# Kernel tuning notes

Measured on AMD Instinct MI355X. Metric: run time of the kernel, lower is better.

## Reference

```python
import jax, jax.numpy as jnp
import numpy as np

SEG = 2048      # segment_length
RATE = 4        # dilated_rate
DIM = 768
LN_EPS = 1e-5


def _sparsify(x):
    # b (l s) d -> b l s d, take every RATE-th within segment, flatten back
    b, L, d = x.shape
    x = x.reshape(b, L // SEG, SEG, d)[:, :, ::RATE]
    return x.reshape(b, -1, d)


def _layernorm(x, gamma, beta):
    mu = jnp.mean(x, axis=-1, keepdims=True)
    var = jnp.mean(jnp.square(x - mu), axis=-1, keepdims=True)
    return (x - mu) / jnp.sqrt(var + LN_EPS) * gamma + beta


def setup_inputs() -> dict:
    key = jax.random.key(0)
    ks = jax.random.split(key, 6)
    B, L, D = 4, 8192, DIM
    return {
        "Q": jax.random.normal(ks[0], (B, L, D), dtype=jnp.float32),
        "K": jax.random.normal(ks[1], (B, L, D), dtype=jnp.float32),
        "V": jax.random.normal(ks[2], (B, L, D), dtype=jnp.float32),
        "Wq": jax.random.normal(ks[3], (D, D), dtype=jnp.float32) * (1.0 / np.sqrt(D)),
        "Wk": jax.random.normal(ks[4], (D, D), dtype=jnp.float32) * (1.0 / np.sqrt(D)),
        "Wv": jax.random.normal(ks[5], (D, D), dtype=jnp.float32) * (1.0 / np.sqrt(D)),
        "ln_gamma": jnp.ones((D,), dtype=jnp.float32),
        "ln_beta": jnp.zeros((D,), dtype=jnp.float32),
    }


def reference(Q, K, V, Wq, Wk, Wv, ln_gamma, ln_beta):
    # strided segment dilation gather
    q = _sparsify(Q)  # [B, Ls, D], Ls = L/SEG * ceil(SEG/RATE)
    k = _sparsify(K)
    v = _sparsify(V)
    # linear projections (torch Linear: y = x @ W.T, no bias)
    q = q @ Wq.T
    k = k @ Wk.T
    v = v @ Wv.T
    # qk LayerNorm (shared norm module)
    q = _layernorm(q, ln_gamma, ln_beta)
    k = _layernorm(k, ln_gamma, ln_beta)
    # scaled dot product attention (non-causal, default scale 1/sqrt(D))
    scale = 1.0 / np.sqrt(q.shape[-1]).astype(np.float32)
    attn = jax.nn.softmax(jnp.einsum('bqd,bkd->bqk', q, k) * scale, axis=-1)
    out = jnp.einsum('bqk,bkd->bqd', attn, v)
    # dropout is identity in eval mode; final softmax over feature dim (as in source)
    return jax.nn.softmax(out, axis=-1)
```

## Files before the change

### kernel.cpp

```cpp
#include <hip/hip_runtime.h>
#include <math.h>

#define SEGLEN 2048
#define SRATE 4
#define DIM 768
#define BATCH 4
#define LFULL 8192
#define LSP 2048
#define NROWS (BATCH * LSP)
#define LN_EPS 1e-5f
#define ATT_SCALE 0.03608439182435161f

typedef __attribute__((ext_vector_type(8))) short s16x8;
typedef __attribute__((ext_vector_type(4))) float f32x4;

__device__ __forceinline__ ushort f2bf(float f) {
    unsigned u = __float_as_uint(f);
    u += 0x7fffu + ((u >> 16) & 1u);
    return (ushort)(u >> 16);
}
__device__ __forceinline__ float bf2f(ushort h) {
    return __uint_as_float(((unsigned)h) << 16);
}

__device__ __forceinline__ void ld_lds16(const ushort* g, ushort* l) {
    __builtin_amdgcn_global_load_lds(
        (const __attribute__((address_space(1))) void*)g,
        (__attribute__((address_space(3))) void*)l, 16, 0, 0);
}

__global__ void pack3(const float* __restrict__ Q, const float* __restrict__ Ks,
                      const float* __restrict__ V, ushort* __restrict__ X) {
    const float* src = blockIdx.z == 0 ? Q : blockIdx.z == 1 ? Ks : V;
    ushort* dst = X + (long)blockIdx.z * (NROWS * DIM);
    int idx = blockIdx.x * 256 + threadIdx.x;
    int r  = idx / (DIM / 4);
    int dg = idx - r * (DIM / 4);
    int bb = r >> 11;
    int s  = r & 2047;
    int seg = s >> 9;
    int j   = s & 511;
    long srow = (long)bb * LFULL + seg * SEGLEN + j * SRATE;
    float4 f = *(const float4*)(src + srow * DIM + dg * 4);
    ushort4 o;
    o.x = f2bf(f.x); o.y = f2bf(f.y); o.z = f2bf(f.z); o.w = f2bf(f.w);
    *(ushort4*)(dst + (long)r * DIM + dg * 4) = o;
}

__global__ void conv3(const float* __restrict__ Wq, const float* __restrict__ Wk,
                      const float* __restrict__ Wv, ushort* __restrict__ W) {
    const float* src = blockIdx.z == 0 ? Wq : blockIdx.z == 1 ? Wk : Wv;
    ushort* dst = W + (long)blockIdx.z * (DIM * DIM);
    int idx = blockIdx.x * 256 + threadIdx.x;
    float4 f = *(const float4*)(src + (long)idx * 4);
    ushort4 o;
    o.x = f2bf(f.x); o.y = f2bf(f.y); o.z = f2bf(f.z); o.w = f2bf(f.w);
    *(ushort4*)(dst + (long)idx * 4) = o;
}

#define GTILE 128
#define GBK 64

template<int MODE>
__global__ __launch_bounds__(256) void gemm_bt(
    const ushort* __restrict__ Ag, const ushort* __restrict__ Bg,
    ushort* __restrict__ Cb, ushort* __restrict__ Cb2,
    float* __restrict__ Cf, float* __restrict__ Cf2, float* __restrict__ lsum,
    int M, int N, int K, int lda, int ldb, long sA, long sB, long sC,
    int ldc, float scale)
{
    __shared__ ushort As[GTILE * GBK];
    __shared__ ushort Bs[GTILE * GBK];

    const int CT = gridDim.x, RT = gridDim.y;
    const int nt = CT * RT;
    const int total = nt * gridDim.z;
    int g = (blockIdx.z * RT + blockIdx.y) * CT + blockIdx.x;
    g = (g & 7) * (total >> 3) + (g >> 3);
    const int z = g / nt;
    const int rem = g - z * nt;
    const int by = rem / CT, bx = rem - by * CT;

    const int bz = (MODE == 3) ? (z >> 1) : z;
    const int hz = (MODE == 3) ? (z & 1) : 0;
    const ushort* A = Ag + (long)bz * sA + (long)hz * K;
    const ushort* B = Bg + (long)bz * sB + (long)hz * K;

    const int tid = threadIdx.x;
    const int rowBase = by * GTILE;
    const int colBase = bx * GTILE;
    const int wid = tid >> 6, lane = tid & 63;
    const int wm = wid >> 1, wn = wid & 1;
    const int quad = lane >> 4, lr = lane & 15;

    f32x4 acc[4][4] = {};

    const ushort* gA = A + (long)(rowBase + wid * 32 + (lane & 7)) * lda + (lane >> 3) * 8;
    const ushort* gB = B + (long)(colBase + wid * 32 + (lane & 7)) * ldb + (lane >> 3) * 8;
    ushort* lA = As + wid * 2048;
    ushort* lB = Bs + wid * 2048;

    const int fra = (wm * 8 + (lr >> 3)) * 512 + (lr & 7) * 8;
    const int frb = (wn * 8 + (lr >> 3)) * 512 + (lr & 7) * 8;

    for (int k0 = 0; k0 < K; k0 += GBK) {
        __syncthreads();
#pragma unroll
        for (int s = 0; s < 4; s++) {
            ld_lds16(gA + (long)s * 8 * lda + k0, lA + s * 512);
            ld_lds16(gB + (long)s * 8 * ldb + k0, lB + s * 512);
        }
        __syncthreads();

#pragma unroll
        for (int h = 0; h < 2; h++) {
            s16x8 af[4], bfm[4];
#pragma unroll
            for (int t = 0; t < 4; t++)
                af[t] = *(const s16x8*)&As[fra + t * 1024 + (h * 4 + quad) * 64];
#pragma unroll
            for (int t = 0; t < 4; t++)
                bfm[t] = *(const s16x8*)&Bs[frb + t * 1024 + (h * 4 + quad) * 64];
#pragma unroll
            for (int i = 0; i < 4; i++)
#pragma unroll
                for (int j = 0; j < 4; j++)
                    acc[i][j] = __builtin_amdgcn_mfma_f32_16x16x32_bf16(af[i], bfm[j], acc[i][j], 0, 0, 0);
        }
    }

    if (MODE == 0) {
        if (z < 2) {
            ushort* Cz = Cb + (long)z * sC;
#pragma unroll
            for (int i = 0; i < 4; i++) {
                int r0 = rowBase + wm * 64 + i * 16 + quad * 4;
#pragma unroll
                for (int j = 0; j < 4; j++) {
                    int c = colBase + wn * 64 + j * 16 + lr;
#pragma unroll
                    for (int reg = 0; reg < 4; reg++)
                        Cz[(long)(r0 + reg) * ldc + c] = f2bf(acc[i][j][reg]);
                }
            }
        } else {
#pragma unroll
            for (int i = 0; i < 4; i++) {
                int r0 = rowBase + wm * 64 + i * 16 + quad * 4;
                int bidx = r0 >> 11;
                int jj = r0 & 2047;
                ushort* Cz = Cb2 + (long)bidx * DIM * LSP;
#pragma unroll
                for (int j = 0; j < 4; j++) {
                    int c = colBase + wn * 64 + j * 16 + lr;
                    ushort4 o;
                    o.x = f2bf(acc[i][j][0]); o.y = f2bf(acc[i][j][1]);
                    o.z = f2bf(acc[i][j][2]); o.w = f2bf(acc[i][j][3]);
                    *(ushort4*)(Cz + (long)c * LSP + jj) = o;
                }
            }
        }
    } else if (MODE == 2) {
        ushort* Cz = Cb + (long)z * sC;
        float* lz = lsum + (long)z * M;
#pragma unroll
        for (int i = 0; i < 4; i++) {
            int r0 = rowBase + wm * 64 + i * 16 + quad * 4;
#pragma unroll
            for (int reg = 0; reg < 4; reg++) {
                float s = 0.f;
#pragma unroll
                for (int j = 0; j < 4; j++) {
                    int c = colBase + wn * 64 + j * 16 + lr;
                    float e = __expf(acc[i][j][reg] * scale);
                    s += e;
                    Cz[(long)(r0 + reg) * ldc + c] = f2bf(e);
                }
                for (int m = 1; m < 16; m <<= 1) s += __shfl_xor(s, m, 64);
                if (lr == 0) atomicAdd(&lz[r0 + reg], s);
            }
        }
    } else {
        float* Cz = (hz ? Cf2 : Cf) + (long)bz * sC;
#pragma unroll
        for (int i = 0; i < 4; i++) {
            int r0 = rowBase + wm * 64 + i * 16 + quad * 4;
#pragma unroll
            for (int j = 0; j < 4; j++) {
                int c = colBase + wn * 64 + j * 16 + lr;
#pragma unroll
                for (int reg = 0; reg < 4; reg++)
                    Cz[(long)(r0 + reg) * ldc + c] = acc[i][j][reg];
            }
        }
    }
}

__global__ __launch_bounds__(256) void ln_inplace(
    ushort* __restrict__ X, const float* __restrict__ gamma,
    const float* __restrict__ beta)
{
    int wid = threadIdx.x >> 6, lane = threadIdx.x & 63;
    int row = blockIdx.x * 4 + wid;
    ushort* xp = X + (long)row * DIM;
    float v[12];
    float s = 0.f;
#pragma unroll
    for (int c = 0; c < 12; c++) { v[c] = bf2f(xp[c * 64 + lane]); s += v[c]; }
    for (int m = 1; m < 64; m <<= 1) s += __shfl_xor(s, m, 64);
    float mean = s * (1.0f / 768.0f);
    float q = 0.f;
#pragma unroll
    for (int c = 0; c < 12; c++) { float d = v[c] - mean; q += d * d; }
    for (int m = 1; m < 64; m <<= 1) q += __shfl_xor(q, m, 64);
    float rstd = rsqrtf(q * (1.0f / 768.0f) + LN_EPS);
#pragma unroll
    for (int c = 0; c < 12; c++) {
        int idx = c * 64 + lane;
        float y = (v[c] - mean) * rstd * gamma[idx] + beta[idx];
        xp[idx] = f2bf(y);
    }
}

__global__ __launch_bounds__(256) void final_softmax(
    const float* __restrict__ O0, const float* __restrict__ O1,
    const float* __restrict__ l, float* __restrict__ out)
{
    int wid = threadIdx.x >> 6, lane = threadIdx.x & 63;
    int row = blockIdx.x * 4 + wid;
    long base = (long)row * DIM;
    float inv = 1.0f / l[row];
    float v[12]; float mx = -1e30f;
#pragma unroll
    for (int c = 0; c < 12; c++) {
        v[c] = (O0[base + c * 64 + lane] + O1[base + c * 64 + lane]) * inv;
        mx = fmaxf(mx, v[c]);
    }
    for (int m = 1; m < 64; m <<= 1) mx = fmaxf(mx, __shfl_xor(mx, m, 64));
    float s = 0.f;
#pragma unroll
    for (int c = 0; c < 12; c++) { v[c] = __expf(v[c] - mx); s += v[c]; }
    for (int m = 1; m < 64; m <<= 1) s += __shfl_xor(s, m, 64);
    float invs = 1.0f / s;
#pragma unroll
    for (int c = 0; c < 12; c++) out[base + c * 64 + lane] = v[c] * invs;
}

extern "C" void kernel_launch(void* const* d_in, const int* in_sizes, int n_in,
                              void* d_out, int out_size, void* d_ws, size_t ws_size,
                              hipStream_t stream)
{
    const float* Q  = (const float*)d_in[0];
    const float* K_ = (const float*)d_in[1];
    const float* V  = (const float*)d_in[2];
    const float* Wq = (const float*)d_in[3];
    const float* Wk = (const float*)d_in[4];
    const float* Wv = (const float*)d_in[5];
    const float* g  = (const float*)d_in[6];
    const float* b  = (const float*)d_in[7];
    float* out = (float*)d_out;

    char* ws = (char*)d_ws;
    ushort* Xq  = (ushort*)(ws + 0);
    ushort* Wqb = (ushort*)(ws + 37748736);
    ushort* qb  = (ushort*)(ws + 41287680);
    ushort* kb  = (ushort*)(ws + 53870592);
    ushort* vT  = (ushort*)(ws + 66453504);
    float*  O0  = (float*)(ws + 79036416);
    float*  l   = (float*)(ws + 104202240);
    ushort* P   = (ushort*)(ws + 0);
    float*  O1  = (float*)(ws + 41287680);

    (void)in_sizes; (void)n_in; (void)out_size; (void)ws_size;

    hipMemsetAsync(l, 0, NROWS * sizeof(float), stream);

    pack3<<<dim3(6144, 1, 3), 256, 0, stream>>>(Q, K_, V, Xq);
    conv3<<<dim3(576, 1, 3), 256, 0, stream>>>(Wq, Wk, Wv, Wqb);

    gemm_bt<0><<<dim3(DIM / GTILE, NROWS / GTILE, 3), 256, 0, stream>>>(
        Xq, Wqb, qb, vT, nullptr, nullptr, nullptr,
        NROWS, DIM, DIM, DIM, DIM,
        (long)NROWS * DIM, (long)DIM * DIM, (long)NROWS * DIM, DIM, 0.f);

    ln_inplace<<<4096, 256, 0, stream>>>(qb, g, b);

    gemm_bt<2><<<dim3(LSP / GTILE, LSP / GTILE, BATCH), 256, 0, stream>>>(
        qb, kb, P, nullptr, nullptr, nullptr, l,
        LSP, LSP, DIM, DIM, DIM,
        (long)LSP * DIM, (long)LSP * DIM, (long)LSP * LSP, LSP, ATT_SCALE);

    gemm_bt<3><<<dim3(DIM / GTILE, LSP / GTILE, BATCH * 2), 256, 0, stream>>>(
        P, vT, nullptr, nullptr, O0, O1, nullptr,
        LSP, DIM, LSP / 2, LSP, LSP,
        (long)LSP * LSP, (long)DIM * LSP, (long)LSP * DIM, DIM, 0.f);

    final_softmax<<<2048, 256, 0, stream>>>(O0, O1, l, out);
}
```

Measured before the change: 460.1 us.

## Double-buffer GEMM LDS tiles and move softmax row sums to separate kernel

The GEMM main loop now uses two LDS buffers with a K-step of 32, issuing the next tile's global-to-LDS loads before computing on the current one. This cuts the barriers per iteration from two to one and lets loads overlap the MFMA work. The atomic row-sum accumulation in the QK^T epilogue, along with its memset, is replaced by a row_sums kernel that re-reads the bf16 P matrix. The trade-off is an extra 32MB read pass and a kernel launch, in exchange for a lighter epilogue with no atomics. The sums are now taken over the bf16-rounded values, which changes rounding slightly.

```diff
diff --git a/kernel.cpp b/kernel.cpp
--- a/kernel.cpp
+++ b/kernel.cpp
@@ -59,18 +59,18 @@
 }
 
 #define GTILE 128
-#define GBK 64
+#define GBK 32
 
 template<int MODE>
 __global__ __launch_bounds__(256) void gemm_bt(
     const ushort* __restrict__ Ag, const ushort* __restrict__ Bg,
     ushort* __restrict__ Cb, ushort* __restrict__ Cb2,
-    float* __restrict__ Cf, float* __restrict__ Cf2, float* __restrict__ lsum,
+    float* __restrict__ Cf, float* __restrict__ Cf2,
     int M, int N, int K, int lda, int ldb, long sA, long sB, long sC,
     int ldc, float scale)
 {
-    __shared__ ushort As[GTILE * GBK];
-    __shared__ ushort Bs[GTILE * GBK];
+    __shared__ ushort As[2 * GTILE * GBK];
+    __shared__ ushort Bs[2 * GTILE * GBK];
 
     const int CT = gridDim.x, RT = gridDim.y;
     const int nt = CT * RT;
@@ -95,38 +95,48 @@
 
     f32x4 acc[4][4] = {};
 
-    const ushort* gA = A + (long)(rowBase + wid * 32 + (lane & 7)) * lda + (lane >> 3) * 8;
-    const ushort* gB = B + (long)(colBase + wid * 32 + (lane & 7)) * ldb + (lane >> 3) * 8;
-    ushort* lA = As + wid * 2048;
-    ushort* lB = Bs + wid * 2048;
-
-    const int fra = (wm * 8 + (lr >> 3)) * 512 + (lr & 7) * 8;
-    const int frb = (wn * 8 + (lr >> 3)) * 512 + (lr & 7) * 8;
-
-    for (int k0 = 0; k0 < K; k0 += GBK) {
+    const int srow = wid * 32 + ((lane >> 5) << 3) + (lane & 7);
+    const int skc  = ((lane >> 3) & 3) * 8;
+    const ushort* gA0 = A + (long)(rowBase + srow) * lda + skc;
+    const ushort* gA1 = A + (long)(rowBase + srow + 16) * lda + skc;
+    const ushort* gB0 = B + (long)(colBase + srow) * ldb + skc;
+    const ushort* gB1 = B + (long)(colBase + srow + 16) * ldb + skc;
+    ushort* lAw = As + wid * 1024;
+    ushort* lBw = Bs + wid * 1024;
+
+    const int fra = (wm * 8 + (lr >> 3)) * 256 + quad * 64 + (lr & 7) * 8;
+    const int frb = (wn * 8 + (lr >> 3)) * 256 + quad * 64 + (lr & 7) * 8;
+
+    const int NI = K / GBK;
+    ld_lds16(gA0, lAw);
+    ld_lds16(gA1, lAw + 512);
+    ld_lds16(gB0, lBw);
+    ld_lds16(gB1, lBw + 512);
+
+    for (int i = 0; i < NI; i++) {
         __syncthreads();
-#pragma unroll
-        for (int s = 0; s < 4; s++) {
-            ld_lds16(gA + (long)s * 8 * lda + k0, lA + s * 512);
-            ld_lds16(gB + (long)s * 8 * ldb + k0, lB + s * 512);
+        if (i + 1 < NI) {
+            const int nb = (i + 1) & 1;
+            const int k0 = (i + 1) * GBK;
+            ld_lds16(gA0 + k0, lAw + nb * 4096);
+            ld_lds16(gA1 + k0, lAw + nb * 4096 + 512);
+            ld_lds16(gB0 + k0, lBw + nb * 4096);
+            ld_lds16(gB1 + k0, lBw + nb * 4096 + 512);
         }
-        __syncthreads();
-
-#pragma unroll
-        for (int h = 0; h < 2; h++) {
-            s16x8 af[4], bfm[4];
-#pragma unroll
-            for (int t = 0; t < 4; t++)
-                af[t] = *(const s16x8*)&As[fra + t * 1024 + (h * 4 + quad) * 64];
-#pragma unroll
-            for (int t = 0; t < 4; t++)
-                bfm[t] = *(const s16x8*)&Bs[frb + t * 1024 + (h * 4 + quad) * 64];
-#pragma unroll
-            for (int i = 0; i < 4; i++)
-#pragma unroll
-                for (int j = 0; j < 4; j++)
-                    acc[i][j] = __builtin_amdgcn_mfma_f32_16x16x32_bf16(af[i], bfm[j], acc[i][j], 0, 0, 0);
-        }
+        const ushort* Ab = As + (i & 1) * 4096;
+        const ushort* Bb = Bs + (i & 1) * 4096;
+        s16x8 af[4], bfm[4];
+#pragma unroll
+        for (int t = 0; t < 4; t++)
+            af[t] = *(const s16x8*)&Ab[fra + t * 512];
+#pragma unroll
+        for (int t = 0; t < 4; t++)
+            bfm[t] = *(const s16x8*)&Bb[frb + t * 512];
+#pragma unroll
+        for (int i2 = 0; i2 < 4; i2++)
+#pragma unroll
+            for (int j = 0; j < 4; j++)
+                acc[i2][j] = __builtin_amdgcn_mfma_f32_16x16x32_bf16(af[i2], bfm[j], acc[i2][j], 0, 0, 0);
     }
 
     if (MODE == 0) {
@@ -162,22 +172,16 @@
         }
     } else if (MODE == 2) {
         ushort* Cz = Cb + (long)z * sC;
-        float* lz = lsum + (long)z * M;
 #pragma unroll
         for (int i = 0; i < 4; i++) {
             int r0 = rowBase + wm * 64 + i * 16 + quad * 4;
 #pragma unroll
-            for (int reg = 0; reg < 4; reg++) {
-                float s = 0.f;
-#pragma unroll
-                for (int j = 0; j < 4; j++) {
-                    int c = colBase + wn * 64 + j * 16 + lr;
-                    float e = __expf(acc[i][j][reg] * scale);
-                    s += e;
-                    Cz[(long)(r0 + reg) * ldc + c] = f2bf(e);
-                }
-                for (int m = 1; m < 16; m <<= 1) s += __shfl_xor(s, m, 64);
-                if (lr == 0) atomicAdd(&lz[r0 + reg], s);
+            for (int j = 0; j < 4; j++) {
+                int c = colBase + wn * 64 + j * 16 + lr;
+#pragma unroll
+                for (int reg = 0; reg < 4; reg++)
+                    Cz[(long)(r0 + reg) * ldc + c] =
+                        f2bf(__expf(acc[i][j][reg] * scale));
             }
         }
     } else {
@@ -194,6 +198,22 @@
             }
         }
     }
+}
+
+__global__ __launch_bounds__(256) void row_sums(
+    const ushort* __restrict__ P, float* __restrict__ l)
+{
+    int wid = threadIdx.x >> 6, lane = threadIdx.x & 63;
+    int row = blockIdx.x * 4 + wid;
+    const ushort* pp = P + (long)row * LSP;
+    float s = 0.f;
+#pragma unroll
+    for (int c = 0; c < 8; c++) {
+        ushort4 u = *(const ushort4*)(pp + (c * 64 + lane) * 4);
+        s += bf2f(u.x) + bf2f(u.y) + bf2f(u.z) + bf2f(u.w);
+    }
+    for (int m = 1; m < 64; m <<= 1) s += __shfl_xor(s, m, 64);
+    if (lane == 0) l[row] = s;
 }
 
 __global__ __launch_bounds__(256) void ln_inplace(
@@ -273,25 +293,25 @@
 
     (void)in_sizes; (void)n_in; (void)out_size; (void)ws_size;
 
-    hipMemsetAsync(l, 0, NROWS * sizeof(float), stream);
-
     pack3<<<dim3(6144, 1, 3), 256, 0, stream>>>(Q, K_, V, Xq);
     conv3<<<dim3(576, 1, 3), 256, 0, stream>>>(Wq, Wk, Wv, Wqb);
 
     gemm_bt<0><<<dim3(DIM / GTILE, NROWS / GTILE, 3), 256, 0, stream>>>(
-        Xq, Wqb, qb, vT, nullptr, nullptr, nullptr,
+        Xq, Wqb, qb, vT, nullptr, nullptr,
         NROWS, DIM, DIM, DIM, DIM,
         (long)NROWS * DIM, (long)DIM * DIM, (long)NROWS * DIM, DIM, 0.f);
 
     ln_inplace<<<4096, 256, 0, stream>>>(qb, g, b);
 
     gemm_bt<2><<<dim3(LSP / GTILE, LSP / GTILE, BATCH), 256, 0, stream>>>(
-        qb, kb, P, nullptr, nullptr, nullptr, l,
+        qb, kb, P, nullptr, nullptr, nullptr,
         LSP, LSP, DIM, DIM, DIM,
         (long)LSP * DIM, (long)LSP * DIM, (long)LSP * LSP, LSP, ATT_SCALE);
 
+    row_sums<<<2048, 256, 0, stream>>>(P, l);
+
     gemm_bt<3><<<dim3(DIM / GTILE, LSP / GTILE, BATCH * 2), 256, 0, stream>>>(
-        P, vT, nullptr, nullptr, O0, O1, nullptr,
+        P, vT, nullptr, nullptr, O0, O1,
         LSP, DIM, LSP / 2, LSP, LSP,
         (long)LSP * LSP, (long)DIM * LSP, (long)LSP * DIM, DIM, 0.f);
 
```

Result: no change. 457.1 us (-0.6%).
